# Optimization experiments

Hardware: AMD Instinct MI355X
Metric: run time of the kernel (lower is better)

Reference implementation:

```python
import jax, jax.numpy as jnp
import numpy as np

N_ATOMS = 50000
DEG = 16
N_EDGES = N_ATOMS * DEG
N_MOL = 1000
NA = 23  # NUMBER_ATOMIC_GRAPH_FEATURES
NB = 7   # NUMBER_BOND_GRAPH_FEATURES


def _sph(v):
    # e3nn-style real spherical harmonics, lmax=2, normalize=False, 'component' normalization
    x, y, z = v[:, 0], v[:, 1], v[:, 2]
    sh1 = jnp.sqrt(3.0) * jnp.stack([x, y, z], axis=-1)  # [E,3] (1o)
    sh2 = jnp.stack([
        jnp.sqrt(15.0) * x * y,
        jnp.sqrt(15.0) * y * z,
        (jnp.sqrt(5.0) / 2.0) * (2 * z * z - x * x - y * y),
        jnp.sqrt(15.0) * x * z,
        (jnp.sqrt(15.0) / 2.0) * (x * x - y * y),
    ], axis=-1)  # [E,5] (2e)
    return sh1, sh2


def setup_inputs() -> dict:
    key = jax.random.key(0)
    ks = jax.random.split(key, 10)
    positions = jax.random.normal(ks[0], (N_ATOMS, 3), jnp.float32)
    x = jax.random.normal(ks[1], (N_ATOMS, NA), jnp.float32)
    edge_attr = jax.random.uniform(ks[2], (N_EDGES, NB), jnp.float32)
    edge_src = jax.random.randint(ks[3], (N_EDGES,), 0, N_ATOMS)
    edge_dst = jnp.repeat(jnp.arange(N_ATOMS), DEG)  # every node has in-degree DEG (required by the module)
    batch = jnp.repeat(jnp.arange(N_MOL), N_ATOMS // N_MOL)
    # tp1: FullyConnectedTensorProduct(NAx0e, 7x0e+7x1o+7x2e -> 32x0e+12x1e+12x1o+8x2e+8x2o)
    # allowed paths: 0e*0e->0e (32), 0e*1o->1o (12), 0e*2e->2e (8); 1e/2o outputs have no path (zero)
    W1_0 = jax.random.normal(ks[4], (NA, NB, 32), jnp.float32)
    W1_1 = jax.random.normal(ks[5], (NA, NB, 12), jnp.float32)
    W1_2 = jax.random.normal(ks[6], (NA, NB, 8), jnp.float32)
    # tp2: paths into 0e: 0e*0e (32x7), 1o*1o (12x7), 2e*2e (8x7)
    W2_0 = jax.random.normal(ks[7], (32, NB, 1), jnp.float32)
    W2_1 = jax.random.normal(ks[8], (12, NB, 1), jnp.float32)
    W2_2 = jax.random.normal(ks[9], (8, NB, 1), jnp.float32)
    return {"positions": positions, "x": x, "edge_attr": edge_attr,
            "W1_0": W1_0, "W1_1": W1_1, "W1_2": W1_2,
            "W2_0": W2_0, "W2_1": W2_1, "W2_2": W2_2,
            "edge_src": edge_src, "edge_dst": edge_dst, "batch": batch}


def reference(positions, x, edge_attr, W1_0, W1_1, W1_2, W2_0, W2_1, W2_2, edge_src, edge_dst, batch):
    N = x.shape[0]
    E = edge_attr.shape[0]
    M = N_MOL
    vec = positions[edge_src] - positions[edge_dst]            # [E,3]
    sh1, sh2 = _sph(vec)
    # FullTensorProduct(7x0e, 0e+1o+2e): scalar block is edge_attr itself; l>0 blocks are outer products
    b1 = edge_attr[:, :, None] * sh1[:, None, :]               # [E,NB,3]
    b2 = edge_attr[:, :, None] * sh2[:, None, :]               # [E,NB,5]
    deg = jax.ops.segment_sum(jnp.ones((E,), positions.dtype), edge_dst, num_segments=N)
    inv_sqrt_deg = 1.0 / jnp.sqrt(deg)                          # all nodes have >=1 edge by construction
    # tp1 on gathered source atom scalars. Since in1 is all-scalar, the SH factor separates:
    t = x[edge_src][:, :, None] * edge_attr[:, None, :]         # [E,NA,NB]
    n1 = 1.0 / np.sqrt(NA * NB)                                 # fan-in normalization
    m0 = jnp.einsum('eab,abo->eo', t, W1_0) * n1                # [E,32] 0e
    m1 = (jnp.einsum('eab,abo->eo', t, W1_1) * n1)[:, :, None] * sh1[:, None, :]  # [E,12,3] 1o
    m2 = (jnp.einsum('eab,abo->eo', t, W1_2) * n1)[:, :, None] * sh2[:, None, :]  # [E,8,5] 2e
    # (tp1's 12x1e and 8x2o outputs are structurally zero and have no path into tp2's 0e output -> dropped)
    s0 = jax.ops.segment_sum(m0, edge_dst, num_segments=N) * inv_sqrt_deg[:, None]
    s1 = jax.ops.segment_sum(m1, edge_dst, num_segments=N) * inv_sqrt_deg[:, None, None]
    s2 = jax.ops.segment_sum(m2, edge_dst, num_segments=N) * inv_sqrt_deg[:, None, None]
    # tp2 -> single 0e; l x l -> 0 contraction is inner product / sqrt(2l+1)
    e0 = jnp.einsum('ea,eb,ab->e', s0[edge_src], edge_attr, W2_0[:, :, 0]) / np.sqrt(32 * NB)
    e1 = jnp.einsum('eam,ebm,ab->e', s1[edge_src], b1, W2_1[:, :, 0]) / (np.sqrt(12 * NB) * np.sqrt(3.0))
    e2 = jnp.einsum('eam,ebm,ab->e', s2[edge_src], b2, W2_2[:, :, 0]) / (np.sqrt(8 * NB) * np.sqrt(5.0))
    edge_out = (e0 + e1 + e2)[:, None]                          # [E,1]
    node_out = jax.ops.segment_sum(edge_out, edge_dst, num_segments=N) * inv_sqrt_deg[:, None]
    apm = jax.ops.segment_sum(jnp.ones((N,), positions.dtype), batch, num_segments=M)
    acc = jax.ops.segment_sum(node_out, batch, num_segments=M)  # [M,1]
    return acc / jnp.sqrt(apm)[:, None]
```

## Files before the change

kernel.cpp:

```cpp
#include <hip/hip_runtime.h>
#include <hip/hip_bf16.h>

#define N_ATOMS 50000
#define DEG 16
#define N_MOL 1000
#define NA 23
#define NB 7
#define O0 32
#define O1 12
#define O2 8
#define OZ 21
#define NT 2
#define ZROW 64
#define NPW 4
#define VFRAG_N 896

typedef __attribute__((ext_vector_type(8))) short short8;
typedef __attribute__((ext_vector_type(4))) float floatx4;

__device__ __forceinline__ unsigned short bfbits(float f) {
    unsigned u = __float_as_uint(f);
    u += 0x7FFFu + ((u >> 16) & 1u);
    return (unsigned short)(u >> 16);
}
__device__ __forceinline__ float bf_lo(unsigned u) { return __uint_as_float(u << 16); }
__device__ __forceinline__ float bf_hi(unsigned u) { return __uint_as_float(u & 0xFFFF0000u); }
__device__ __forceinline__ float wred4(float v) {
    v += __shfl_xor(v, 16, 64); v += __shfl_xor(v, 32, 64); return v;
}

__global__ void k_prep(const float* __restrict__ W1_0, const float* __restrict__ W1_1,
                       const float* __restrict__ W1_2,
                       const float* __restrict__ W2_0, const float* __restrict__ W2_1,
                       const float* __restrict__ W2_2,
                       const float* __restrict__ x, const float* __restrict__ pos,
                       unsigned short* __restrict__ Vfrag,
                       unsigned short* __restrict__ x_bf, float4* __restrict__ pos4,
                       float* __restrict__ out) {
    int idx = blockIdx.x * 256 + threadIdx.x;
    if (idx < N_MOL) out[idx] = 0.0f;
    if (idx < VFRAG_N * 8) {
        int j    = idx & 7;
        int lane = (idx >> 3) & 63;
        int st   = idx >> 9;
        int s = st >> 1, t = st & 1;
        int a = (lane >> 4) * 8 + j, o = t * 16 + (lane & 15);
        float val = 0.f;
        if (a < NA && o < OZ) {
            const float n1 = 0.07881104062391006f;
            const float q  = 0.25f;
            float acc = 0.f;
            if (o < 7) {
                const float c0 = 0.06681531047810609f;
                const float* w1 = W1_0 + (a * NB + s) * O0;
                for (int k = 0; k < O0; k++) acc += w1[k] * W2_0[k * NB + o];
                val = acc * (n1 * c0 * q);
            } else if (o < 14) {
                const float c1 = 0.06299407883487121f;
                const float* w1 = W1_1 + (a * NB + s) * O1;
                for (int k = 0; k < O1; k++) acc += w1[k] * W2_1[k * NB + (o - 7)];
                val = acc * (n1 * c1 * q);
            } else {
                const float c2 = 0.05976143046671968f;
                const float* w1 = W1_2 + (a * NB + s) * O2;
                for (int k = 0; k < O2; k++) acc += w1[k] * W2_2[k * NB + (o - 14)];
                val = acc * (n1 * c2 * q);
            }
        }
        Vfrag[idx] = bfbits(val);
    }
    if (idx < N_ATOMS) {
        float4 p; p.x = pos[idx * 3 + 0]; p.y = pos[idx * 3 + 1];
        p.z = pos[idx * 3 + 2]; p.w = 0.f;
        pos4[idx] = p;
    }
    if (idx < N_ATOMS * 32) {
        int n = idx >> 5, a = idx & 31;
        x_bf[idx] = bfbits((a < NA) ? x[n * NA + a] : 0.f);
    }
}

__global__ __launch_bounds__(256, 5) void k2_s(const float4* __restrict__ pos4,
        const unsigned short* __restrict__ x_bf, const float* __restrict__ edge_attr,
        const int* __restrict__ edge_src, const unsigned short* __restrict__ Vfrag,
        unsigned short* __restrict__ zbuf) {
    __shared__ short8 wfrag[VFRAG_N];
    __shared__ float hbuf[4][16][8];
    const int tid  = threadIdx.x;
    const int wid  = tid >> 6;
    const int lane = tid & 63;
    const int lcol = lane & 15;
    const int quad = lane >> 4;

    {
        uint4* dst = (uint4*)wfrag;
        const uint4* src4 = (const uint4*)Vfrag;
        for (int i = tid; i < VFRAG_N; i += 256) dst[i] = src4[i];
    }
    __syncthreads();

    const int wgid = __builtin_amdgcn_readfirstlane(blockIdx.x * 4 + wid);
    const int base = wgid * NPW;
    if (base >= N_ATOMS) return;

    float (*hb)[8] = hbuf[wid];
    const float s3 = 1.7320508075688772f, s15 = 3.872983346207417f;
    const float s5h = 1.118033988749895f, s15h = 1.9364916731037085f;

    auto clampn = [&](int i) { int nn = base + i; return nn < N_ATOMS ? nn : N_ATOMS - 1; };
    int s0v = edge_src[clampn(0) * DEG + lcol];
    int s1v = edge_src[clampn(1) * DEG + lcol];
    uint4 xu0 = *(const uint4*)(x_bf + s0v * 32 + quad * 8);
    float4 pp0 = pos4[s0v];
    float e0v[NB];
    {
        const float* p = edge_attr + ((size_t)clampn(0) * DEG + lcol) * NB;
        #pragma unroll
        for (int b = 0; b < NB; b++) e0v[b] = p[b];
    }

    #pragma unroll 1
    for (int i = 0; i < NPW; i++) {
        const int n = base + i;
        if (n >= N_ATOMS) break;
        int s2v = edge_src[clampn(i + 2 < NPW ? i + 2 : i) * DEG + lcol];
        uint4 xu1 = *(const uint4*)(x_bf + s1v * 32 + quad * 8);
        float4 pp1 = pos4[s1v];
        float e1v[NB];
        {
            const float* p = edge_attr + ((size_t)clampn(i + 1 < NPW ? i + 1 : i) * DEG + lcol) * NB;
            #pragma unroll
            for (int b = 0; b < NB; b++) e1v[b] = p[b];
        }
        float xf[8];
        xf[0] = bf_lo(xu0.x); xf[1] = bf_hi(xu0.x);
        xf[2] = bf_lo(xu0.y); xf[3] = bf_hi(xu0.y);
        xf[4] = bf_lo(xu0.z); xf[5] = bf_hi(xu0.z);
        xf[6] = bf_lo(xu0.w); xf[7] = bf_hi(xu0.w);

        const float4 pd = pos4[n];
        if (lane < 16) {
            const float vx = pp0.x - pd.x, vy = pp0.y - pd.y, vz = pp0.z - pd.z;
            hb[lane][0] = s3 * vx;  hb[lane][1] = s3 * vy;  hb[lane][2] = s3 * vz;
            hb[lane][3] = s15 * vx * vy;
            hb[lane][4] = s15 * vy * vz;
            hb[lane][5] = s5h * (2.f * vz * vz - vx * vx - vy * vy);
            hb[lane][6] = s15 * vx * vz;
            hb[lane][7] = s15h * (vx * vx - vy * vy);
        }
        floatx4 acc0 = {0.f,0.f,0.f,0.f}, acc1 = {0.f,0.f,0.f,0.f};
        #pragma unroll
        for (int s = 0; s < 7; s++) {
            const float eb = e0v[s];
            union { short8 v; unsigned u[4]; } af;
            #pragma unroll
            for (int j = 0; j < 8; j += 2) {
                float2 pr; pr.x = xf[j] * eb; pr.y = xf[j + 1] * eb;
                __hip_bfloat162 bb = __float22bfloat162_rn(pr);
                af.u[j >> 1] = *(unsigned*)&bb;
            }
            acc0 = __builtin_amdgcn_mfma_f32_16x16x32_bf16(af.v, wfrag[(s*NT+0)*64 + lane], acc0, 0, 0, 0);
            acc1 = __builtin_amdgcn_mfma_f32_16x16x32_bf16(af.v, wfrag[(s*NT+1)*64 + lane], acc1, 0, 0, 0);
        }
        float4 hA[4], hB[4];
        #pragma unroll
        for (int r = 0; r < 4; r++) {
            int e = quad * 4 + r;
            hA[r] = *(const float4*)&hb[e][0];
            hB[r] = *(const float4*)&hb[e][4];
        }
        unsigned short* sr = zbuf + (size_t)n * ZROW;
        const bool useA = (lcol >= 14);
        float v0 = acc0[0] + acc0[1] + acc0[2] + acc0[3];
        float u0 = 0.f, u1 = 0.f, u2 = 0.f;
        float t0 = 0.f, t1 = 0.f, t2 = 0.f, t3 = 0.f, t4 = 0.f;
        #pragma unroll
        for (int r = 0; r < 4; r++) {
            float m0 = acc0[r], m1 = acc1[r];
            u0 += m0 * hA[r].x; u1 += m0 * hA[r].y; u2 += m0 * hA[r].z;
            float mz = useA ? m0 : m1;
            t0 += mz * hA[r].w; t1 += mz * hB[r].x; t2 += mz * hB[r].y;
            t3 += mz * hB[r].z; t4 += mz * hB[r].w;
        }
        v0 = wred4(v0);
        u0 = wred4(u0); u1 = wred4(u1); u2 = wred4(u2);
        t0 = wred4(t0); t1 = wred4(t1); t2 = wred4(t2); t3 = wred4(t3); t4 = wred4(t4);
        if (quad == 0) {
            if (lcol < 7) sr[lcol * 8] = bfbits(v0);
            else if (lcol < 14) {
                int b = lcol - 7;
                sr[b * 8 + 1] = bfbits(u0); sr[b * 8 + 2] = bfbits(u1); sr[b * 8 + 3] = bfbits(u2);
            }
            if (lcol >= 14 || lcol < 5) {
                int b = useA ? (lcol - 14) : (lcol + 2);
                sr[b * 8 + 4] = bfbits(t0); sr[b * 8 + 5] = bfbits(t1); sr[b * 8 + 6] = bfbits(t2);
                sr[b * 8 + 7] = bfbits(t3); sr[56 + b] = bfbits(t4);
            }
            if (lcol == 5) sr[63] = 0;
        }
        s0v = s1v; s1v = s2v;
        xu0 = xu1; pp0 = pp1;
        #pragma unroll
        for (int b = 0; b < NB; b++) e0v[b] = e1v[b];
    }
}

__global__ __launch_bounds__(256, 6) void k3_fused(const float4* __restrict__ pos4,
        const float* __restrict__ edge_attr, const int* __restrict__ edge_src,
        const unsigned short* __restrict__ zbuf, float* __restrict__ out) {
    const int tid  = threadIdx.x;
    const int wid  = tid >> 6;
    const int lane = tid & 63;
    const int g    = lane >> 4;
    const int k    = lane & 15;
    const int n = __builtin_amdgcn_readfirstlane(blockIdx.x * 4 + wid) * 4 + g;

    const int s = edge_src[n * DEG + k];
    const uint4* zr = (const uint4*)(zbuf + (size_t)s * ZROW);
    uint4 zq[8];
    #pragma unroll
    for (int i = 0; i < 8; i++) zq[i] = zr[i];

    const float* eap = edge_attr + ((size_t)n * DEG + k) * NB;
    float4 e03 = *(const float4*)(eap);
    float2 e45 = *(const float2*)(eap + 4);
    float  e6  = eap[6];

    const float4 ps = pos4[s];
    const float4 pd = pos4[n];
    const float vx = ps.x - pd.x, vy = ps.y - pd.y, vz = ps.z - pd.z;
    const float s3 = 1.7320508075688772f, s15 = 3.872983346207417f;
    const float s5h = 1.118033988749895f, s15h = 1.9364916731037085f;
    const float h1 = s3 * vx, h2 = s3 * vy, h3 = s3 * vz;
    const float h4 = s15 * vx * vy, h5 = s15 * vy * vz;
    const float h6 = s5h * (2.f * vz * vz - vx * vx - vy * vy);
    const float h7 = s15 * vx * vz, h8 = s15h * (vx * vx - vy * vy);

    float eab[NB] = {e03.x, e03.y, e03.z, e03.w, e45.x, e45.y, e6};
    float c8v[NB];
    c8v[0] = bf_lo(zq[7].x); c8v[1] = bf_hi(zq[7].x);
    c8v[2] = bf_lo(zq[7].y); c8v[3] = bf_hi(zq[7].y);
    c8v[4] = bf_lo(zq[7].z); c8v[5] = bf_hi(zq[7].z);
    c8v[6] = bf_lo(zq[7].w);

    float acc = 0.f;
    #pragma unroll
    for (int b = 0; b < NB; b++) {
        const uint4 z = zq[b];
        float t = bf_lo(z.x)
                + h1 * bf_hi(z.x) + h2 * bf_lo(z.y) + h3 * bf_hi(z.y)
                + h4 * bf_lo(z.z) + h5 * bf_hi(z.z) + h6 * bf_lo(z.w)
                + h7 * bf_hi(z.w) + h8 * c8v[b];
        acc += eab[b] * t;
    }

    acc += __shfl_xor(acc, 1, 64);
    acc += __shfl_xor(acc, 2, 64);
    acc += __shfl_xor(acc, 4, 64);
    acc += __shfl_xor(acc, 8, 64);
    if (k == 0)
        atomicAdd(out + n / 50, acc * 0.035355339059327376f);
}

extern "C" void kernel_launch(void* const* d_in, const int* in_sizes, int n_in,
                              void* d_out, int out_size, void* d_ws, size_t ws_size,
                              hipStream_t stream) {
    const float* pos  = (const float*)d_in[0];
    const float* x    = (const float*)d_in[1];
    const float* ea   = (const float*)d_in[2];
    const float* W1_0 = (const float*)d_in[3];
    const float* W1_1 = (const float*)d_in[4];
    const float* W1_2 = (const float*)d_in[5];
    const float* W2_0 = (const float*)d_in[6];
    const float* W2_1 = (const float*)d_in[7];
    const float* W2_2 = (const float*)d_in[8];
    const int*   esrc = (const int*)d_in[9];
    float* out = (float*)d_out;

    char* ws = (char*)d_ws;
    unsigned short* Vfrag = (unsigned short*)ws;
    unsigned short* zbuf  = (unsigned short*)(ws + 32768);
    unsigned short* x_bf  = (unsigned short*)(ws + 32768 + 6400000);
    float4*         pos4  = (float4*)(ws + 32768 + 6400000 + 3200000);

    hipLaunchKernelGGL(k_prep, dim3((N_ATOMS * 32 + 255) / 256), dim3(256), 0, stream,
                       W1_0, W1_1, W1_2, W2_0, W2_1, W2_2, x, pos, Vfrag, x_bf, pos4, out);
    hipLaunchKernelGGL(k2_s, dim3((N_ATOMS / NPW + 3) / 4), dim3(256), 0, stream,
                       pos4, x_bf, ea, esrc, Vfrag, zbuf);
    hipLaunchKernelGGL(k3_fused, dim3(N_ATOMS / 16), dim3(256), 0, stream,
                       pos4, ea, esrc, zbuf, out);
}
```

Measured before the change: 184.9 us.

## Remap final edge kernel to 8 lanes per edge, one row chunk each

The final per-edge contraction kernel now gives each edge 8 lanes. Each lane loads one 16-byte chunk of the source node's z row and one edge_attr element, instead of one lane loading the whole 128-byte row. The ninth coefficient is shared through cross-lane shuffles, and a full-wave reduction replaces the 16-lane one. The aim is more coalesced, parallel memory access and lower register pressure (launch bounds raised to 8), at the cost of 8x more threads, more redundant spherical-harmonic arithmetic per lane, and twice as many atomics per node.

```diff
diff --git a/kernel.cpp b/kernel.cpp
--- a/kernel.cpp
+++ b/kernel.cpp
@@ -2,6 +2,7 @@
 #include <hip/hip_bf16.h>
 
 #define N_ATOMS 50000
+#define N_EDGES 800000
 #define DEG 16
 #define N_MOL 1000
 #define NA 23
@@ -205,26 +206,22 @@
     }
 }
 
-__global__ __launch_bounds__(256, 6) void k3_fused(const float4* __restrict__ pos4,
+__global__ __launch_bounds__(256, 8) void k3_g(const float4* __restrict__ pos4,
         const float* __restrict__ edge_attr, const int* __restrict__ edge_src,
         const unsigned short* __restrict__ zbuf, float* __restrict__ out) {
     const int tid  = threadIdx.x;
     const int wid  = tid >> 6;
     const int lane = tid & 63;
-    const int g    = lane >> 4;
-    const int k    = lane & 15;
-    const int n = __builtin_amdgcn_readfirstlane(blockIdx.x * 4 + wid) * 4 + g;
-
-    const int s = edge_src[n * DEG + k];
-    const uint4* zr = (const uint4*)(zbuf + (size_t)s * ZROW);
-    uint4 zq[8];
-    #pragma unroll
-    for (int i = 0; i < 8; i++) zq[i] = zr[i];
-
-    const float* eap = edge_attr + ((size_t)n * DEG + k) * NB;
-    float4 e03 = *(const float4*)(eap);
-    float2 e45 = *(const float2*)(eap + 4);
-    float  e6  = eap[6];
+    const int g    = lane >> 3;
+    const int r    = lane & 7;
+    const int wgid = __builtin_amdgcn_readfirstlane(blockIdx.x * 4 + wid);
+    const int ebase = wgid * 8;
+    const int n = ebase >> 4;
+
+    const int e = ebase + g;
+    const int s = edge_src[e];
+    const uint4 zq = *(const uint4*)(zbuf + (size_t)s * ZROW + r * 8);
+    const float eav = (r < NB) ? edge_attr[(size_t)e * NB + r] : 0.f;
 
     const float4 ps = pos4[s];
     const float4 pd = pos4[n];
@@ -236,29 +233,25 @@
     const float h6 = s5h * (2.f * vz * vz - vx * vx - vy * vy);
     const float h7 = s15 * vx * vz, h8 = s15h * (vx * vx - vy * vy);
 
-    float eab[NB] = {e03.x, e03.y, e03.z, e03.w, e45.x, e45.y, e6};
-    float c8v[NB];
-    c8v[0] = bf_lo(zq[7].x); c8v[1] = bf_hi(zq[7].x);
-    c8v[2] = bf_lo(zq[7].y); c8v[3] = bf_hi(zq[7].y);
-    c8v[4] = bf_lo(zq[7].z); c8v[5] = bf_hi(zq[7].z);
-    c8v[6] = bf_lo(zq[7].w);
-
-    float acc = 0.f;
+    const int src7 = lane | 7;
+    const unsigned w0 = (unsigned)__shfl((int)zq.x, src7, 64);
+    const unsigned w1 = (unsigned)__shfl((int)zq.y, src7, 64);
+    const unsigned w2 = (unsigned)__shfl((int)zq.z, src7, 64);
+    const unsigned w3 = (unsigned)__shfl((int)zq.w, src7, 64);
+    const unsigned wa = (r & 4) ? w2 : w0;
+    const unsigned wb = (r & 4) ? w3 : w1;
+    const unsigned wc = (r & 2) ? wb : wa;
+    const float c8 = (r & 1) ? bf_hi(wc) : bf_lo(wc);
+
+    float t = bf_lo(zq.x)
+            + h1 * bf_hi(zq.x) + h2 * bf_lo(zq.y) + h3 * bf_hi(zq.y)
+            + h4 * bf_lo(zq.z) + h5 * bf_hi(zq.z) + h6 * bf_lo(zq.w)
+            + h7 * bf_hi(zq.w) + h8 * c8;
+    float acc = eav * t;
+
     #pragma unroll
-    for (int b = 0; b < NB; b++) {
-        const uint4 z = zq[b];
-        float t = bf_lo(z.x)
-                + h1 * bf_hi(z.x) + h2 * bf_lo(z.y) + h3 * bf_hi(z.y)
-                + h4 * bf_lo(z.z) + h5 * bf_hi(z.z) + h6 * bf_lo(z.w)
-                + h7 * bf_hi(z.w) + h8 * c8v[b];
-        acc += eab[b] * t;
-    }
-
-    acc += __shfl_xor(acc, 1, 64);
-    acc += __shfl_xor(acc, 2, 64);
-    acc += __shfl_xor(acc, 4, 64);
-    acc += __shfl_xor(acc, 8, 64);
-    if (k == 0)
+    for (int off = 32; off >= 1; off >>= 1) acc += __shfl_xor(acc, off, 64);
+    if (lane == 0)
         atomicAdd(out + n / 50, acc * 0.035355339059327376f);
 }
 
@@ -287,6 +280,6 @@
                        W1_0, W1_1, W1_2, W2_0, W2_1, W2_2, x, pos, Vfrag, x_bf, pos4, out);
     hipLaunchKernelGGL(k2_s, dim3((N_ATOMS / NPW + 3) / 4), dim3(256), 0, stream,
                        pos4, x_bf, ea, esrc, Vfrag, zbuf);
-    hipLaunchKernelGGL(k3_fused, dim3(N_ATOMS / 16), dim3(256), 0, stream,
+    hipLaunchKernelGGL(k3_g, dim3(N_EDGES / 8 / 4), dim3(256), 0, stream,
                        pos4, ea, esrc, zbuf, out);
 }
```

Result: slower. 265.7 us (+43.7%).
